# Performance work log

Measured on AMD Instinct MI355X. Metric: run time of the kernel, lower is better.

The kernel has to match this reference:

```python
import jax, jax.numpy as jnp
import numpy as np

N = 50000   # nodes
E = 800000  # directed edges
IN = 128
H = 128


def setup_inputs() -> dict:
    key = jax.random.key(0)
    k1, k2, k3, k4 = jax.random.split(key, 4)
    x = jax.random.normal(k1, (N, IN), jnp.float32)
    edge_index = jax.random.randint(k2, (2, E), 0, N, jnp.int32)
    W1 = jax.random.normal(k3, (IN, H), jnp.float32) / np.sqrt(IN)
    b1 = jnp.zeros((H,), jnp.float32)
    W2 = jax.random.normal(k4, (H, H), jnp.float32) / np.sqrt(H)
    b2 = jnp.zeros((H,), jnp.float32)
    return {"x": x, "edge_index": edge_index, "W1": W1, "b1": b1, "W2": W2, "b2": b2}


def _gcn_norm(edge_index, num_nodes):
    # PyG GCNConv default: add self-loops, symmetric normalization D^-1/2 A D^-1/2
    row, col = edge_index[0], edge_index[1]
    loop = jnp.arange(num_nodes, dtype=row.dtype)
    row = jnp.concatenate([row, loop])
    col = jnp.concatenate([col, loop])
    deg = jax.ops.segment_sum(jnp.ones_like(row, jnp.float32), row, num_segments=num_nodes)
    dinv = jnp.where(deg > 0, jax.lax.rsqrt(deg), 0.0)
    norm = dinv[row] * dinv[col]  # [E + N]
    return row, col, norm


def _gcn_conv(x, W, b, row, col, norm, num_nodes):
    xw = x @ W                                  # [N, H] dense GEMM
    msg = norm[:, None] * xw[col]               # gather + scale, [E+N, H]
    out = jax.ops.segment_sum(msg, row, num_segments=num_nodes)  # scatter-add
    return out + b


def reference(x, edge_index, W1, b1, W2, b2):
    row, col, norm = _gcn_norm(edge_index, N)
    h = _gcn_conv(x, W1, b1, row, col, norm, N)
    h = jax.nn.relu(h)
    out = _gcn_conv(h, W2, b2, row, col, norm, N)
    return out
```

## Files before the change

kernel.cpp:

```cpp
#include <hip/hip_runtime.h>

#define NN 50000
#define NE 800000
#define HD 128
#define NBK 98
#define BCAP 16384
#define FB 196
#define CVB 200

using short8 = __attribute__((ext_vector_type(8))) short;
using f32x4  = __attribute__((ext_vector_type(4))) float;

__device__ inline unsigned short rne_bf16(float v) {
    union { float f; unsigned u; } c; c.f = v;
    return (unsigned short)((c.u + 0x7fff + ((c.u >> 16) & 1)) >> 16);
}
__device__ inline float bf16_to_f32(unsigned short h) {
    union { unsigned u; float f; } c; c.u = ((unsigned)h) << 16;
    return c.f;
}


__global__ __launch_bounds__(256) void k_fill1(const int* __restrict__ ei,
                                               int* __restrict__ bcur,
                                               int* __restrict__ pairs,
                                               const float* __restrict__ W1,
                                               const float* __restrict__ W2,
                                               unsigned short* __restrict__ hi1,
                                               unsigned short* __restrict__ lo1,
                                               unsigned short* __restrict__ hi2,
                                               unsigned short* __restrict__ lo2,
                                               const float* __restrict__ x,
                                               unsigned short* __restrict__ xb) {
    int t = threadIdx.x, b = blockIdx.x;
    if (b >= FB + 16) {
        int bb = b - (FB + 16);
        const int total = NN * HD / 8;
        for (int i = bb * 256 + t; i < total; i += CVB * 256) {
            float4 a0 = ((const float4*)x)[i * 2];
            float4 a1 = ((const float4*)x)[i * 2 + 1];
            short8 r;
            r[0] = (short)rne_bf16(a0.x); r[1] = (short)rne_bf16(a0.y);
            r[2] = (short)rne_bf16(a0.z); r[3] = (short)rne_bf16(a0.w);
            r[4] = (short)rne_bf16(a1.x); r[5] = (short)rne_bf16(a1.y);
            r[6] = (short)rne_bf16(a1.z); r[7] = (short)rne_bf16(a1.w);
            *(short8*)(xb + (size_t)i * 8) = r;
        }
        return;
    }
    if (b >= FB) {
        int bb = b - FB;
        const float* W = (bb < 8) ? W1 : W2;
        unsigned short* hi = (bb < 8) ? hi1 : hi2;
        unsigned short* lo = (bb < 8) ? lo1 : lo2;
        int tid = (bb & 7) * 256 + t;
        int lane = tid & 63;
        int ks = (tid >> 6) & 3;
        int nt = tid >> 8;
        int n = nt * 16 + (lane & 15);
        int k0 = ks * 32 + (lane >> 4) * 8;
#pragma unroll
        for (int j = 0; j < 8; ++j) {
            float v = W[(k0 + j) * HD + n];
            unsigned short h = rne_bf16(v);
            float rem = v - bf16_to_f32(h);
            hi[(size_t)tid * 8 + j] = h;
            lo[(size_t)tid * 8 + j] = rne_bf16(rem);
        }
        return;
    }
    __shared__ int dr[4096], sc[4096];
    __shared__ int hist[NBK], base[NBK];
    for (int i = t; i < NBK; i += 256) hist[i] = 0;
    __syncthreads();
    int e0 = b * 4096;
#pragma unroll
    for (int u = 0; u < 16; ++u) {
        int idx = u * 256 + t, e = e0 + idx;
        int r = -1, c = 0;
        if (e < NE) {
            r = ei[e];
            c = ei[NE + e];
            atomicAdd(&hist[r >> 9], 1);
        }
        dr[idx] = r;
        sc[idx] = c;
    }
    __syncthreads();
    for (int i = t; i < NBK; i += 256) {
        base[i] = atomicAdd(&bcur[i], hist[i]);
        hist[i] = 0;
    }
    __syncthreads();
#pragma unroll
    for (int u = 0; u < 16; ++u) {
        int idx = u * 256 + t;
        int r = dr[idx];
        if (r >= 0) {
            int bk = r >> 9;
            int pos = atomicAdd(&hist[bk], 1);
            pairs[(size_t)bk * BCAP + base[bk] + pos] = ((r & 511) << 16) | sc[idx];
        }
    }
}


__global__ __launch_bounds__(256) void k_fill2(const int* __restrict__ pairs,
                                               const int* __restrict__ bcur,
                                               int* __restrict__ deg,
                                               int* __restrict__ offs,
                                               float* __restrict__ dinv,
                                               int* __restrict__ csr) {
    __shared__ int spart[256];
    __shared__ int cnt[512];
    __shared__ int lcur[512];
    int b = blockIdx.x, t = threadIdx.x;
    int n0 = b * 512;
    int nodes = min(512, NN - n0);

    int v = (t < NBK && t < b) ? bcur[t] : 0;
    spart[t] = v;
    __syncthreads();
#pragma unroll
    for (int o = 128; o > 0; o >>= 1) {
        if (t < o) spart[t] += spart[t + o];
        __syncthreads();
    }
    int base = spart[0];
    int tot = bcur[b];

    for (int i = t; i < 512; i += 256) cnt[i] = 0;
    __syncthreads();
    const int* pp = pairs + (size_t)b * BCAP;
    for (int p = t; p < tot; p += 256) atomicAdd(&cnt[pp[p] >> 16], 1);
    __syncthreads();

    int d0 = (2 * t < nodes) ? cnt[2 * t] : 0;
    int d1 = (2 * t + 1 < nodes) ? cnt[2 * t + 1] : 0;
    spart[t] = d0 + d1;
    __syncthreads();
#pragma unroll
    for (int o = 1; o < 256; o <<= 1) {
        int x = (t >= o) ? spart[t - o] : 0;
        __syncthreads();
        spart[t] += x;
        __syncthreads();
    }
    int excl = spart[t] - (d0 + d1);
    int o0 = base + excl, o1 = o0 + d0;
    if (2 * t < nodes) {
        offs[n0 + 2 * t] = o0;
        lcur[2 * t] = o0;
        deg[n0 + 2 * t] = d0;
        dinv[n0 + 2 * t] = rsqrtf((float)(d0 + 1));
    }
    if (2 * t + 1 < nodes) {
        offs[n0 + 2 * t + 1] = o1;
        lcur[2 * t + 1] = o1;
        deg[n0 + 2 * t + 1] = d1;
        dinv[n0 + 2 * t + 1] = rsqrtf((float)(d1 + 1));
    }
    __syncthreads();

    for (int p = t; p < tot; p += 256) {
        int pr = pp[p];
        int slot = atomicAdd(&lcur[pr >> 16], 1);
        csr[slot] = pr & 0xFFFF;
    }
}


template <bool RELU, bool OUTBF16>
__global__ __launch_bounds__(256) void k_agg_gemm(const unsigned short* __restrict__ src,
                                                  const int* __restrict__ csr,
                                                  const int* __restrict__ offs,
                                                  const int* __restrict__ deg,
                                                  const float* __restrict__ dinv,
                                                  const unsigned short* __restrict__ Whi,
                                                  const unsigned short* __restrict__ Wlo,
                                                  const float* __restrict__ bias,
                                                  void* __restrict__ Cout) {
    __shared__ unsigned short As[16 * 128];
    int t = threadIdx.x;
    int w = t >> 6, l = t & 63;
    int q = l >> 4, sub = l & 15;
    int n0 = blockIdx.x * 16;

#pragma unroll
    for (int i = 0; i < 4; ++i) {
        int row = w * 4 + i;
        int node = n0 + row;
        int o = offs[node];
        int dg = deg[node];
        float d = dinv[node];

        float acc[8];
        if (q == 0) {
            float s = d * d;
            short8 v = *(const short8*)(src + (size_t)node * HD + sub * 8);
#pragma unroll
            for (int k = 0; k < 8; ++k) acc[k] = s * bf16_to_f32((unsigned short)v[k]);
        } else {
#pragma unroll
            for (int k = 0; k < 8; ++k) acc[k] = 0.0f;
        }

        for (int base = 0; base < dg; base += 64) {
            int n = min(64, dg - base);
            int myc = (l < n) ? csr[o + base + l] : node;
            float myw = (l < n) ? d * dinv[myc] : 0.0f;
            int jmax = (n + 15) >> 4;
            for (int j = 0; j < jmax; ++j) {
                int e = j * 16 + q;
                int c0 = __shfl(myc, e);
                int c1 = __shfl(myc, e + 4);
                int c2 = __shfl(myc, e + 8);
                int c3 = __shfl(myc, e + 12);
                float w0 = __shfl(myw, e);
                float w1 = __shfl(myw, e + 4);
                float w2 = __shfl(myw, e + 8);
                float w3 = __shfl(myw, e + 12);
                short8 v0 = *(const short8*)(src + (size_t)c0 * HD + sub * 8);
                short8 v1 = *(const short8*)(src + (size_t)c1 * HD + sub * 8);
                short8 v2 = *(const short8*)(src + (size_t)c2 * HD + sub * 8);
                short8 v3 = *(const short8*)(src + (size_t)c3 * HD + sub * 8);
#pragma unroll
                for (int k = 0; k < 8; ++k) {
                    acc[k] = fmaf(w0, bf16_to_f32((unsigned short)v0[k]), acc[k]);
                    acc[k] = fmaf(w1, bf16_to_f32((unsigned short)v1[k]), acc[k]);
                    acc[k] = fmaf(w2, bf16_to_f32((unsigned short)v2[k]), acc[k]);
                    acc[k] = fmaf(w3, bf16_to_f32((unsigned short)v3[k]), acc[k]);
                }
            }
        }
#pragma unroll
        for (int k = 0; k < 8; ++k) {
            acc[k] += __shfl_xor(acc[k], 16);
            acc[k] += __shfl_xor(acc[k], 32);
        }
        if (q == 0) {
            short8 r;
#pragma unroll
            for (int k = 0; k < 8; ++k) r[k] = (short)rne_bf16(acc[k]);
            int byte = (sub * 16) ^ ((row & 7) << 4);
            *(short8*)((char*)As + row * 256 + byte) = r;
        }
    }
    __syncthreads();

    f32x4 cacc[2];
    cacc[0] = (f32x4){0.f, 0.f, 0.f, 0.f};
    cacc[1] = (f32x4){0.f, 0.f, 0.f, 0.f};
    int arow = l & 15;
#pragma unroll
    for (int ks = 0; ks < 4; ++ks) {
        int byte = (ks * 64 + (l >> 4) * 16) ^ ((arow & 7) << 4);
        short8 ahi = *(const short8*)((char*)As + arow * 256 + byte);
#pragma unroll
        for (int i = 0; i < 2; ++i) {
            int nt = w * 2 + i;
            size_t fo = ((size_t)(nt * 4 + ks) * 64 + l) * 8;
            short8 bhi = *(const short8*)(Whi + fo);
            short8 blo = *(const short8*)(Wlo + fo);
            cacc[i] = __builtin_amdgcn_mfma_f32_16x16x32_bf16(ahi, bhi, cacc[i], 0, 0, 0);
            cacc[i] = __builtin_amdgcn_mfma_f32_16x16x32_bf16(ahi, blo, cacc[i], 0, 0, 0);
        }
    }

#pragma unroll
    for (int i = 0; i < 2; ++i) {
        int nt = w * 2 + i;
        int col = nt * 16 + (l & 15);
        float bv = bias[col];
#pragma unroll
        for (int r = 0; r < 4; ++r) {
            int gr = n0 + (l >> 4) * 4 + r;
            float v = cacc[i][r] + bv;
            if (RELU) v = fmaxf(v, 0.f);
            if (OUTBF16)
                ((unsigned short*)Cout)[(size_t)gr * HD + col] = rne_bf16(v);
            else
                ((float*)Cout)[(size_t)gr * HD + col] = v;
        }
    }
}


extern "C" void kernel_launch(void* const* d_in, const int* in_sizes, int n_in,
                              void* d_out, int out_size, void* d_ws, size_t ws_size,
                              hipStream_t stream) {
    const float* x  = (const float*)d_in[0];
    const int*   ei = (const int*)d_in[1];
    const float* W1 = (const float*)d_in[2];
    const float* b1 = (const float*)d_in[3];
    const float* W2 = (const float*)d_in[4];
    const float* b2 = (const float*)d_in[5];
    float* out = (float*)d_out;

    char* ws = (char*)d_ws;
    size_t off = 0;
    auto alloc = [&](size_t bytes) {
        void* p = ws + off;
        off = (off + bytes + 255) & ~(size_t)255;
        return p;
    };
    int*   bcur = (int*)alloc(NBK * 4);
    int*   deg  = (int*)alloc(NN * 4);
    int*   offs = (int*)alloc(NN * 4);
    float* dinv = (float*)alloc(NN * 4);
    int*   csr  = (int*)alloc((size_t)NE * 4);
    unsigned short* xb = (unsigned short*)alloc((size_t)NN * HD * 2);
    char* region = (char*)alloc((size_t)NN * HD * 2);
    int*  pairs = (int*)region;
    unsigned short* hb = (unsigned short*)region;
    unsigned short* Whi1 = (unsigned short*)alloc(16384 * 2);
    unsigned short* Wlo1 = (unsigned short*)alloc(16384 * 2);
    unsigned short* Whi2 = (unsigned short*)alloc(16384 * 2);
    unsigned short* Wlo2 = (unsigned short*)alloc(16384 * 2);

    hipMemsetAsync(bcur, 0, NBK * 4, stream);
    k_fill1<<<FB + 16 + CVB, 256, 0, stream>>>(ei, bcur, pairs, W1, W2,
                                               Whi1, Wlo1, Whi2, Wlo2, x, xb);
    k_fill2<<<NBK, 256, 0, stream>>>(pairs, bcur, deg, offs, dinv, csr);

    k_agg_gemm<true, true><<<NN / 16, 256, 0, stream>>>(xb, csr, offs, deg, dinv,
                                                        Whi1, Wlo1, b1, hb);
    k_agg_gemm<false, false><<<NN / 16, 256, 0, stream>>>(hb, csr, offs, deg, dinv,
                                                          Whi2, Wlo2, b2, out);
}
```

Measured before the change: 199.2 us.

## Use 8 waves per block, each aggregating two nodes with interleaved gathers

The fused aggregate+GEMM kernel now launches 512 threads, so each of 8 wavefronts aggregates two node rows instead of four sequentially. The two rows' neighbor gathers are interleaved in one loop to raise memory-level parallelism, and each wave computes one 16-column MFMA tile. This aims to hide gather latency through more concurrent loads and waves, at the cost of higher register pressure and some divergence when the two rows have different degrees.

```diff
diff --git a/kernel.cpp b/kernel.cpp
--- a/kernel.cpp
+++ b/kernel.cpp
@@ -171,7 +171,7 @@
 
 
 template <bool RELU, bool OUTBF16>
-__global__ __launch_bounds__(256) void k_agg_gemm(const unsigned short* __restrict__ src,
+__global__ __launch_bounds__(512) void k_agg_gemm(const unsigned short* __restrict__ src,
                                                   const int* __restrict__ csr,
                                                   const int* __restrict__ offs,
                                                   const int* __restrict__ deg,
@@ -186,102 +186,153 @@
     int q = l >> 4, sub = l & 15;
     int n0 = blockIdx.x * 16;
 
-#pragma unroll
-    for (int i = 0; i < 4; ++i) {
-        int row = w * 4 + i;
-        int node = n0 + row;
-        int o = offs[node];
-        int dg = deg[node];
-        float d = dinv[node];
-
-        float acc[8];
-        if (q == 0) {
-            float s = d * d;
-            short8 v = *(const short8*)(src + (size_t)node * HD + sub * 8);
-#pragma unroll
-            for (int k = 0; k < 8; ++k) acc[k] = s * bf16_to_f32((unsigned short)v[k]);
-        } else {
-#pragma unroll
-            for (int k = 0; k < 8; ++k) acc[k] = 0.0f;
-        }
-
-        for (int base = 0; base < dg; base += 64) {
-            int n = min(64, dg - base);
-            int myc = (l < n) ? csr[o + base + l] : node;
-            float myw = (l < n) ? d * dinv[myc] : 0.0f;
-            int jmax = (n + 15) >> 4;
-            for (int j = 0; j < jmax; ++j) {
-                int e = j * 16 + q;
-                int c0 = __shfl(myc, e);
-                int c1 = __shfl(myc, e + 4);
-                int c2 = __shfl(myc, e + 8);
-                int c3 = __shfl(myc, e + 12);
-                float w0 = __shfl(myw, e);
-                float w1 = __shfl(myw, e + 4);
-                float w2 = __shfl(myw, e + 8);
-                float w3 = __shfl(myw, e + 12);
-                short8 v0 = *(const short8*)(src + (size_t)c0 * HD + sub * 8);
-                short8 v1 = *(const short8*)(src + (size_t)c1 * HD + sub * 8);
-                short8 v2 = *(const short8*)(src + (size_t)c2 * HD + sub * 8);
-                short8 v3 = *(const short8*)(src + (size_t)c3 * HD + sub * 8);
-#pragma unroll
-                for (int k = 0; k < 8; ++k) {
-                    acc[k] = fmaf(w0, bf16_to_f32((unsigned short)v0[k]), acc[k]);
-                    acc[k] = fmaf(w1, bf16_to_f32((unsigned short)v1[k]), acc[k]);
-                    acc[k] = fmaf(w2, bf16_to_f32((unsigned short)v2[k]), acc[k]);
-                    acc[k] = fmaf(w3, bf16_to_f32((unsigned short)v3[k]), acc[k]);
-                }
+    int rowA = w * 2, rowB = w * 2 + 1;
+    int nodeA = n0 + rowA, nodeB = n0 + rowB;
+    int oA = offs[nodeA], oB = offs[nodeB];
+    int dgA = deg[nodeA], dgB = deg[nodeB];
+    float dA = dinv[nodeA], dB = dinv[nodeB];
+
+    int nA = min(64, dgA), nB = min(64, dgB);
+    int mycA = (l < nA) ? csr[oA + l] : nodeA;
+    int mycB = (l < nB) ? csr[oB + l] : nodeB;
+    float mywA = (l < nA) ? dA * dinv[mycA] : 0.0f;
+    float mywB = (l < nB) ? dB * dinv[mycB] : 0.0f;
+
+    float accA[8], accB[8];
+    if (q == 0) {
+        float sA = dA * dA, sB = dB * dB;
+        short8 vA = *(const short8*)(src + (size_t)nodeA * HD + sub * 8);
+        short8 vB = *(const short8*)(src + (size_t)nodeB * HD + sub * 8);
+#pragma unroll
+        for (int k = 0; k < 8; ++k) {
+            accA[k] = sA * bf16_to_f32((unsigned short)vA[k]);
+            accB[k] = sB * bf16_to_f32((unsigned short)vB[k]);
+        }
+    } else {
+#pragma unroll
+        for (int k = 0; k < 8; ++k) { accA[k] = 0.0f; accB[k] = 0.0f; }
+    }
+
+    int jmA = (nA + 15) >> 4, jmB = (nB + 15) >> 4;
+    int jm = max(jmA, jmB);
+    for (int j = 0; j < jm; ++j) {
+        int e = j * 16 + q;
+        bool doA = (j < jmA), doB = (j < jmB);
+        short8 vA0, vA1, vA2, vA3, vB0, vB1, vB2, vB3;
+        float wA0, wA1, wA2, wA3, wB0, wB1, wB2, wB3;
+        if (doA) {
+            int c0 = __shfl(mycA, e), c1 = __shfl(mycA, e + 4);
+            int c2 = __shfl(mycA, e + 8), c3 = __shfl(mycA, e + 12);
+            wA0 = __shfl(mywA, e); wA1 = __shfl(mywA, e + 4);
+            wA2 = __shfl(mywA, e + 8); wA3 = __shfl(mywA, e + 12);
+            vA0 = *(const short8*)(src + (size_t)c0 * HD + sub * 8);
+            vA1 = *(const short8*)(src + (size_t)c1 * HD + sub * 8);
+            vA2 = *(const short8*)(src + (size_t)c2 * HD + sub * 8);
+            vA3 = *(const short8*)(src + (size_t)c3 * HD + sub * 8);
+        }
+        if (doB) {
+            int c0 = __shfl(mycB, e), c1 = __shfl(mycB, e + 4);
+            int c2 = __shfl(mycB, e + 8), c3 = __shfl(mycB, e + 12);
+            wB0 = __shfl(mywB, e); wB1 = __shfl(mywB, e + 4);
+            wB2 = __shfl(mywB, e + 8); wB3 = __shfl(mywB, e + 12);
+            vB0 = *(const short8*)(src + (size_t)c0 * HD + sub * 8);
+            vB1 = *(const short8*)(src + (size_t)c1 * HD + sub * 8);
+            vB2 = *(const short8*)(src + (size_t)c2 * HD + sub * 8);
+            vB3 = *(const short8*)(src + (size_t)c3 * HD + sub * 8);
+        }
+        if (doA) {
+#pragma unroll
+            for (int k = 0; k < 8; ++k) {
+                accA[k] = fmaf(wA0, bf16_to_f32((unsigned short)vA0[k]), accA[k]);
+                accA[k] = fmaf(wA1, bf16_to_f32((unsigned short)vA1[k]), accA[k]);
+                accA[k] = fmaf(wA2, bf16_to_f32((unsigned short)vA2[k]), accA[k]);
+                accA[k] = fmaf(wA3, bf16_to_f32((unsigned short)vA3[k]), accA[k]);
             }
         }
+        if (doB) {
+#pragma unroll
+            for (int k = 0; k < 8; ++k) {
+                accB[k] = fmaf(wB0, bf16_to_f32((unsigned short)vB0[k]), accB[k]);
+                accB[k] = fmaf(wB1, bf16_to_f32((unsigned short)vB1[k]), accB[k]);
+                accB[k] = fmaf(wB2, bf16_to_f32((unsigned short)vB2[k]), accB[k]);
+                accB[k] = fmaf(wB3, bf16_to_f32((unsigned short)vB3[k]), accB[k]);
+            }
+        }
+    }
+
+    for (int base = 64; base < dgA; base += 64) {
+        int n = min(64, dgA - base);
+        int myc = (l < n) ? csr[oA + base + l] : nodeA;
+        float myw = (l < n) ? dA * dinv[myc] : 0.0f;
+        for (int j2 = 0; j2 * 4 < n; ++j2) {
+            int c = __shfl(myc, j2 * 4 + q);
+            float wg = __shfl(myw, j2 * 4 + q);
+            short8 v = *(const short8*)(src + (size_t)c * HD + sub * 8);
+#pragma unroll
+            for (int k = 0; k < 8; ++k)
+                accA[k] = fmaf(wg, bf16_to_f32((unsigned short)v[k]), accA[k]);
+        }
+    }
+    for (int base = 64; base < dgB; base += 64) {
+        int n = min(64, dgB - base);
+        int myc = (l < n) ? csr[oB + base + l] : nodeB;
+        float myw = (l < n) ? dB * dinv[myc] : 0.0f;
+        for (int j2 = 0; j2 * 4 < n; ++j2) {
+            int c = __shfl(myc, j2 * 4 + q);
+            float wg = __shfl(myw, j2 * 4 + q);
+            short8 v = *(const short8*)(src + (size_t)c * HD + sub * 8);
+#pragma unroll
+            for (int k = 0; k < 8; ++k)
+                accB[k] = fmaf(wg, bf16_to_f32((unsigned short)v[k]), accB[k]);
+        }
+    }
+
+#pragma unroll
+    for (int k = 0; k < 8; ++k) {
+        accA[k] += __shfl_xor(accA[k], 16);
+        accA[k] += __shfl_xor(accA[k], 32);
+        accB[k] += __shfl_xor(accB[k], 16);
+        accB[k] += __shfl_xor(accB[k], 32);
+    }
+    if (q == 0) {
+        short8 rA, rB;
 #pragma unroll
         for (int k = 0; k < 8; ++k) {
-            acc[k] += __shfl_xor(acc[k], 16);
-            acc[k] += __shfl_xor(acc[k], 32);
-        }
-        if (q == 0) {
-            short8 r;
-#pragma unroll
-            for (int k = 0; k < 8; ++k) r[k] = (short)rne_bf16(acc[k]);
-            int byte = (sub * 16) ^ ((row & 7) << 4);
-            *(short8*)((char*)As + row * 256 + byte) = r;
-        }
-    }
-    __syncthreads();
-
-    f32x4 cacc[2];
-    cacc[0] = (f32x4){0.f, 0.f, 0.f, 0.f};
-    cacc[1] = (f32x4){0.f, 0.f, 0.f, 0.f};
+            rA[k] = (short)rne_bf16(accA[k]);
+            rB[k] = (short)rne_bf16(accB[k]);
+        }
+        int byteA = (sub * 16) ^ ((rowA & 7) << 4);
+        int byteB = (sub * 16) ^ ((rowB & 7) << 4);
+        *(short8*)((char*)As + rowA * 256 + byteA) = rA;
+        *(short8*)((char*)As + rowB * 256 + byteB) = rB;
+    }
+    __syncthreads();
+
+    f32x4 cacc = (f32x4){0.f, 0.f, 0.f, 0.f};
     int arow = l & 15;
+    int nt = w;
 #pragma unroll
     for (int ks = 0; ks < 4; ++ks) {
         int byte = (ks * 64 + (l >> 4) * 16) ^ ((arow & 7) << 4);
         short8 ahi = *(const short8*)((char*)As + arow * 256 + byte);
-#pragma unroll
-        for (int i = 0; i < 2; ++i) {
-            int nt = w * 2 + i;
-            size_t fo = ((size_t)(nt * 4 + ks) * 64 + l) * 8;
-            short8 bhi = *(const short8*)(Whi + fo);
-            short8 blo = *(const short8*)(Wlo + fo);
-            cacc[i] = __builtin_amdgcn_mfma_f32_16x16x32_bf16(ahi, bhi, cacc[i], 0, 0, 0);
-            cacc[i] = __builtin_amdgcn_mfma_f32_16x16x32_bf16(ahi, blo, cacc[i], 0, 0, 0);
-        }
-    }
-
-#pragma unroll
-    for (int i = 0; i < 2; ++i) {
-        int nt = w * 2 + i;
-        int col = nt * 16 + (l & 15);
-        float bv = bias[col];
-#pragma unroll
-        for (int r = 0; r < 4; ++r) {
-            int gr = n0 + (l >> 4) * 4 + r;
-            float v = cacc[i][r] + bv;
-            if (RELU) v = fmaxf(v, 0.f);
-            if (OUTBF16)
-                ((unsigned short*)Cout)[(size_t)gr * HD + col] = rne_bf16(v);
-            else
-                ((float*)Cout)[(size_t)gr * HD + col] = v;
-        }
+        size_t fo = ((size_t)(nt * 4 + ks) * 64 + l) * 8;
+        short8 bhi = *(const short8*)(Whi + fo);
+        short8 blo = *(const short8*)(Wlo + fo);
+        cacc = __builtin_amdgcn_mfma_f32_16x16x32_bf16(ahi, bhi, cacc, 0, 0, 0);
+        cacc = __builtin_amdgcn_mfma_f32_16x16x32_bf16(ahi, blo, cacc, 0, 0, 0);
+    }
+
+    int col = nt * 16 + (l & 15);
+    float bv = bias[col];
+#pragma unroll
+    for (int r = 0; r < 4; ++r) {
+        int gr = n0 + (l >> 4) * 4 + r;
+        float v = cacc[r] + bv;
+        if (RELU) v = fmaxf(v, 0.f);
+        if (OUTBF16)
+            ((unsigned short*)Cout)[(size_t)gr * HD + col] = rne_bf16(v);
+        else
+            ((float*)Cout)[(size_t)gr * HD + col] = v;
     }
 }
 
@@ -323,8 +374,8 @@
                                                Whi1, Wlo1, Whi2, Wlo2, x, xb);
     k_fill2<<<NBK, 256, 0, stream>>>(pairs, bcur, deg, offs, dinv, csr);
 
-    k_agg_gemm<true, true><<<NN / 16, 256, 0, stream>>>(xb, csr, offs, deg, dinv,
+    k_agg_gemm<true, true><<<NN / 16, 512, 0, stream>>>(xb, csr, offs, deg, dinv,
                                                         Whi1, Wlo1, b1, hb);
-    k_agg_gemm<false, false><<<NN / 16, 256, 0, stream>>>(hb, csr, offs, deg, dinv,
+    k_agg_gemm<false, false><<<NN / 16, 512, 0, stream>>>(hb, csr, offs, deg, dinv,
                                                           Whi2, Wlo2, b2, out);
 }
```

New measurement: 211.9 us. 1.06x slower.
